# Performance work log

Hardware: AMD Instinct MI355X
Metric: run time of the kernel (lower is better)

Reference implementation:

```python
import jax, jax.numpy as jnp
import numpy as np

N_NODES = 50000
N_EDGES = 600000
D_IN = 128
D_HID = 128
N_IDX = 4096


def gcn_conv(x, W, b, edge_index, num_nodes):
    """PyG GCNConv: add self loops, symmetric deg normalization, scatter-add, bias."""
    h = x @ W  # [N, D_out]
    loop = jnp.arange(num_nodes, dtype=edge_index.dtype)
    src = jnp.concatenate([edge_index[0], loop])
    dst = jnp.concatenate([edge_index[1], loop])
    deg = jax.ops.segment_sum(jnp.ones_like(dst, dtype=h.dtype), dst, num_segments=num_nodes)
    dinv = jnp.where(deg > 0, jax.lax.rsqrt(jnp.maximum(deg, 1.0)), 0.0)
    norm = dinv[src] * dinv[dst]  # [E+N]
    msgs = h[src] * norm[:, None]
    out = jax.ops.segment_sum(msgs, dst, num_segments=num_nodes)
    return out + b


def setup_inputs() -> dict:
    key = jax.random.key(0)
    ks = jax.random.split(key, 18)
    d = {
        "x": jax.random.normal(ks[0], (N_NODES, D_IN), dtype=jnp.float32),
        "syntactic_edge_index": jax.random.randint(ks[1], (2, N_EDGES), 0, N_NODES, dtype=jnp.int32),
        "sequential_edge_index": jax.random.randint(ks[2], (2, N_EDGES), 0, N_NODES, dtype=jnp.int32),
        "semantic_edge_index": jax.random.randint(ks[3], (2, N_EDGES), 0, N_NODES, dtype=jnp.int32),
        "index": jax.random.randint(ks[4], (N_IDX,), 0, N_NODES, dtype=jnp.int32),
    }
    s = 1.0 / np.sqrt(D_IN)
    names = ["syn", "seq", "sem"]
    for i, n in enumerate(names):
        d[f"w1_{n}"] = jax.random.uniform(ks[5 + i], (D_IN, D_HID), jnp.float32, -s, s)
        d[f"b1_{n}"] = jnp.zeros((D_HID,), jnp.float32)
        d[f"w2_{n}"] = jax.random.uniform(ks[8 + i], (D_HID, D_HID), jnp.float32, -s, s)
        d[f"b2_{n}"] = jnp.zeros((D_HID,), jnp.float32)
    return d


def reference(x, syntactic_edge_index, sequential_edge_index, semantic_edge_index, index,
              w1_syn, b1_syn, w1_seq, b1_seq, w1_sem, b1_sem,
              w2_syn, b2_syn, w2_seq, b2_seq, w2_sem, b2_sem):
    n = x.shape[0]
    # layer 1: three parallel GCN branches + ReLU (dropout is identity in eval mode)
    a = jax.nn.relu(gcn_conv(x, w1_syn, b1_syn, syntactic_edge_index, n))
    b = jax.nn.relu(gcn_conv(x, w1_seq, b1_seq, sequential_edge_index, n))
    c = jax.nn.relu(gcn_conv(x, w1_sem, b1_sem, semantic_edge_index, n))
    h = jnp.maximum(jnp.maximum(a, b), c)
    # layer 2
    a2 = jax.nn.relu(gcn_conv(h, w2_syn, b2_syn, syntactic_edge_index, n))
    b2 = jax.nn.relu(gcn_conv(h, w2_seq, b2_seq, sequential_edge_index, n))
    c2 = jax.nn.relu(gcn_conv(h, w2_sem, b2_sem, semantic_edge_index, n))
    out = jnp.maximum(jnp.maximum(a2, b2), c2)
    return out[index]
```

## Files before the change

### kernel.cpp

```cpp
#include <hip/hip_runtime.h>
#include <hip/hip_fp16.h>

#define NN 50000
#define NE 600000
#define NG 3
#define D  128
#define NI 4096
#define BW 1024
#define NBUCK 49
#define CAP 16384
#define REGION (NBUCK * CAP)
#define EPT_BIN 16
#define EPB_BIN (256 * EPT_BIN)
#define NBLK_BIN ((NE + EPB_BIN - 1) / EPB_BIN)
#define XCVT_BLKS 3125
#define WCVT_BLKS 48

typedef _Float16 half8 __attribute__((ext_vector_type(8)));
typedef float floatx4 __attribute__((ext_vector_type(4)));

static __device__ __forceinline__ float wextract(unsigned int v) {
  unsigned short u = (unsigned short)(v >> 16);
  _Float16 h;
  __builtin_memcpy(&h, &u, 2);
  return (float)h;
}

static __device__ __forceinline__ unsigned short h16(float f) {
  _Float16 h = (_Float16)f;
  unsigned short u;
  __builtin_memcpy(&u, &h, 2);
  return u;
}


__global__ __launch_bounds__(256) void prep_kernel(
    const float* __restrict__ x, __half* __restrict__ xh,
    const float* __restrict__ W0, const float* __restrict__ W1, const float* __restrict__ W2,
    const float* __restrict__ W3, const float* __restrict__ W4, const float* __restrict__ W5,
    __half* __restrict__ Wf, int* __restrict__ gcur) {
  int blk = blockIdx.x;
  int tid = threadIdx.x;
  if (blk < XCVT_BLKS) {
    int i = blk * 256 + tid;
    size_t base = (size_t)i * 8;
    float4 v0 = *(const float4*)&x[base];
    float4 v1 = *(const float4*)&x[base + 4];
    half8 h;
    h[0] = (_Float16)v0.x; h[1] = (_Float16)v0.y; h[2] = (_Float16)v0.z; h[3] = (_Float16)v0.w;
    h[4] = (_Float16)v1.x; h[5] = (_Float16)v1.y; h[6] = (_Float16)v1.z; h[7] = (_Float16)v1.w;
    *(half8*)&xh[base] = h;
  } else if (blk < XCVT_BLKS + WCVT_BLKS) {
    const float* Wm[6] = {W0, W1, W2, W3, W4, W5};
    int t = (blk - XCVT_BLKS) * 256 + tid;
    int mat = t >> 11;
    int fr = (t >> 6) & 31;
    int lane = t & 63;
    int tt = fr >> 2, ks = fr & 3;
    int n = tt * 16 + (lane & 15);
    int kb = ks * 32 + (lane >> 4) * 8;
    const float* W = Wm[mat];
#pragma unroll
    for (int j = 0; j < 8; j++)
      Wf[(size_t)t * 8 + j] = __float2half(W[(kb + j) * 128 + n]);
  } else {
    if (tid < NG * NBUCK) gcur[tid] = (tid % NBUCK) * CAP;
  }
}

__global__ __launch_bounds__(256) void bin_kernel(const int* __restrict__ e0,
    const int* __restrict__ e1, const int* __restrict__ e2,
    int* __restrict__ gcur, unsigned int* __restrict__ binned) {
  __shared__ int cnt[4][NBUCK];
  __shared__ int base[NBUCK];
  __shared__ int woff[4][NBUCK];
  int g = blockIdx.y;
  const int* ei = (g == 0) ? e0 : ((g == 1) ? e1 : e2);
  int tid = threadIdx.x;
  int wave = tid >> 6;
  if (tid < NBUCK) { cnt[0][tid] = 0; cnt[1][tid] = 0; cnt[2][tid] = 0; cnt[3][tid] = 0; }
  __syncthreads();
  int estart = blockIdx.x * EPB_BIN;
  int src[EPT_BIN], dst[EPT_BIN], rk[EPT_BIN];
#pragma unroll
  for (int i = 0; i < EPT_BIN; i++) {
    int e = estart + tid + i * 256;
    if (e < NE) {
      src[i] = ei[e];
      dst[i] = ei[NE + e];
      rk[i] = atomicAdd(&cnt[wave][dst[i] >> 10], 1);
    } else {
      rk[i] = -1;
    }
  }
  __syncthreads();
  if (tid < NBUCK) {
    int c0 = cnt[0][tid], c1 = cnt[1][tid], c2 = cnt[2][tid], c3 = cnt[3][tid];
    int total = c0 + c1 + c2 + c3;
    base[tid] = (total > 0) ? atomicAdd(&gcur[g * NBUCK + tid], total) : 0;
    woff[0][tid] = 0; woff[1][tid] = c0; woff[2][tid] = c0 + c1; woff[3][tid] = c0 + c1 + c2;
  }
  __syncthreads();
#pragma unroll
  for (int i = 0; i < EPT_BIN; i++) {
    if (rk[i] >= 0) {
      int b = dst[i] >> 10;
      int pos = base[b] + woff[wave][b] + rk[i];
      if (pos < (b + 1) * CAP)
        binned[(size_t)g * REGION + pos] =
            (unsigned int)src[i] | ((unsigned int)dst[i] << 16);
    }
  }
}

__global__ __launch_bounds__(256) void csr_kernel(const unsigned int* __restrict__ binned,
    const int* __restrict__ gcur, unsigned int* __restrict__ rp32,
    float* __restrict__ dinv, unsigned short* __restrict__ dinvh) {
  __shared__ int deg[BW];
  __shared__ int wsum[4];
  int g = blockIdx.y, b = blockIdx.x;
  int tid = threadIdx.x;
  int node0 = b * BW;
  int cbase = b * CAP;
  int total = min(gcur[g * NBUCK + b] - cbase, CAP);
  const unsigned int* bp = binned + (size_t)g * REGION + cbase;
  for (int i = tid; i < BW; i += 256) deg[i] = 0;
  __syncthreads();
  for (int e = tid; e < total; e += 256) {
    unsigned int p = bp[e];
    atomicAdd(&deg[(int)(p >> 16) - node0], 1);
  }
  __syncthreads();
  int d0 = deg[tid * 4], d1 = deg[tid * 4 + 1], d2 = deg[tid * 4 + 2], d3 = deg[tid * 4 + 3];
  int s = d0 + d1 + d2 + d3;
  int lane = tid & 63;
  int incl = s;
#pragma unroll
  for (int off = 1; off < 64; off <<= 1) {
    int n = __shfl_up(incl, off, 64);
    if (lane >= off) incl += n;
  }
  if (lane == 63) wsum[tid >> 6] = incl;
  __syncthreads();
  int wbase = 0;
#pragma unroll
  for (int w = 0; w < 4; w++)
    if (w < (tid >> 6)) wbase += wsum[w];
  int ex = wbase + incl - s;
  int exs[4] = {ex, ex + d0, ex + d0 + d1, ex + d0 + d1 + d2};
  int ds[4] = {d0, d1, d2, d3};
#pragma unroll
  for (int k = 0; k < 4; k++) {
    int node = node0 + tid * 4 + k;
    if (node < NN) {
      unsigned int st = (unsigned int)(cbase + exs[k]);
      rp32[g * NN + node] = st | ((unsigned int)ds[k] << 20);
      float di = rsqrtf((float)ds[k] + 1.0f);
      dinv[g * NN + node] = di;
      dinvh[g * NN + node] = h16(di);
    }
  }
}

__global__ __launch_bounds__(256) void fillp_kernel(const unsigned int* __restrict__ binned,
    const int* __restrict__ gcur, const unsigned int* __restrict__ rp32,
    const unsigned short* __restrict__ dinvh, unsigned int* __restrict__ colp) {
  __shared__ int cur[BW];
  int g = blockIdx.y, b = blockIdx.x;
  int tid = threadIdx.x;
  int node0 = b * BW;
  int cbase = b * CAP;
  int total = min(gcur[g * NBUCK + b] - cbase, CAP);
  const unsigned int* bp = binned + (size_t)g * REGION + cbase;
  for (int i = tid; i < BW; i += 256) {
    int node = node0 + i;
    cur[i] = (node < NN) ? (int)(rp32[g * NN + node] & 0xFFFFFu) : 0;
  }
  __syncthreads();
  const unsigned short* dh = dinvh + (size_t)g * NN;
  unsigned int* cg = colp + (size_t)g * REGION;
  for (int e = tid; e < total; e += 256) {
    unsigned int p = bp[e];
    int srcid = (int)(p & 0xffffu);
    int r = atomicAdd(&cur[(int)(p >> 16) - node0], 1);
    cg[r] = (unsigned int)srcid | ((unsigned int)dh[srcid] << 16);
  }
}


__global__ __launch_bounds__(256) void aggb_kernel(
    const __half* __restrict__ srch, const unsigned int* __restrict__ rp32,
    const unsigned int* __restrict__ colp, const float* __restrict__ dinv,
    const int* __restrict__ index, __half* __restrict__ tout, int nrows) {
  int b = blockIdx.y;
  int lane = threadIdx.x & 63;
  int grp = lane >> 4;
  int l16 = lane & 15;
  int gb = grp << 4;
  int wv = (blockIdx.x * 256 + threadIdx.x) >> 6;
  int w = wv * 4 + grp;
  int valid = (w < nrows);
  int wc = valid ? w : 0;
  int node = index ? index[wc] : wc;
  const _Float16* srcv = (const _Float16*)srch;
  unsigned int r32 = rp32[(size_t)b * NN + node];
  int s = (int)(r32 & 0xFFFFFu);
  int n = valid ? (int)(r32 >> 20) : 0;
  float di = dinv[b * NN + node];
  half8 selfh = *(const half8*)&srcv[(size_t)node * D + l16 * 8];
  float a[8];
#pragma unroll
  for (int k = 0; k < 8; k++) a[k] = di * (float)selfh[k];
  int nmax = n;
  nmax = max(nmax, __shfl_xor(nmax, 16, 64));
  nmax = max(nmax, __shfl_xor(nmax, 32, 64));
  const unsigned int* cp = colp + (size_t)b * REGION;
  for (int j0 = 0; j0 < nmax; j0 += 16) {
    unsigned int c = (j0 + l16 < n) ? cp[s + j0 + l16] : 0u;
    int rem = nmax - j0;
    rem = (rem > 16) ? 16 : rem;
    for (int jj = 0; jj < rem; jj += 4) {
      unsigned int v0 = (unsigned int)__shfl((int)c, gb + jj + 0, 64);
      unsigned int v1 = (unsigned int)__shfl((int)c, gb + jj + 1, 64);
      unsigned int v2 = (unsigned int)__shfl((int)c, gb + jj + 2, 64);
      unsigned int v3 = (unsigned int)__shfl((int)c, gb + jj + 3, 64);
      half8 h0 = *(const half8*)&srcv[(size_t)(v0 & 0xffffu) * D + l16 * 8];
      half8 h1 = *(const half8*)&srcv[(size_t)(v1 & 0xffffu) * D + l16 * 8];
      half8 h2 = *(const half8*)&srcv[(size_t)(v2 & 0xffffu) * D + l16 * 8];
      half8 h3 = *(const half8*)&srcv[(size_t)(v3 & 0xffffu) * D + l16 * 8];
      float w0 = wextract(v0), w1 = wextract(v1);
      float w2 = wextract(v2), w3 = wextract(v3);
#pragma unroll
      for (int k = 0; k < 8; k++) a[k] = fmaf((float)h0[k], w0, a[k]);
#pragma unroll
      for (int k = 0; k < 8; k++) a[k] = fmaf((float)h1[k], w1, a[k]);
#pragma unroll
      for (int k = 0; k < 8; k++) a[k] = fmaf((float)h2[k], w2, a[k]);
#pragma unroll
      for (int k = 0; k < 8; k++) a[k] = fmaf((float)h3[k], w3, a[k]);
    }
  }
  if (valid) {
    half8 o;
#pragma unroll
    for (int k = 0; k < 8; k++) o[k] = (_Float16)(di * a[k]);
    _Float16* tv = (_Float16*)tout;
    *(half8*)&tv[(size_t)b * nrows * D + (size_t)w * D + l16 * 8] = o;
  }
}


#define ALD 136

__global__ __launch_bounds__(256) void mmf_kernel(const __half* __restrict__ A,
    const __half* __restrict__ Wf,
    const float* __restrict__ B0, const float* __restrict__ B1, const float* __restrict__ B2,
    __half* __restrict__ outh, float* __restrict__ outf, int M) {
  __shared__ _Float16 As[128 * ALD];
  __shared__ _Float16 Ws[16384];
  const float* Bb[3] = {B0, B1, B2};
  const int tid = threadIdx.x;
  const int wave = tid >> 6, lane = tid & 63;
  const int wr = (wave >> 1) * 64, wc = (wave & 1) * 64;
  const int ln = lane & 15, quad = lane >> 4;
  const int row0 = blockIdx.x * 128;
  float om[4][4][4];

  for (int b = 0; b < 3; b++) {
    const __half* Wb = Wf + (size_t)b * 16384;
#pragma unroll
    for (int i = 0; i < 8; i++) {
      int id = tid + i * 256;
      *(half8*)&Ws[id * 8] = *(const half8*)&Wb[(size_t)id * 8];
    }
    const __half* Ab = A + (size_t)b * M * D;
#pragma unroll
    for (int i = 0; i < 8; i++) {
      int idx = tid + i * 256;
      int r = idx >> 4, c8 = idx & 15;
      int gr = row0 + r;
      gr = (gr < M) ? gr : (M - 1);
      half8 v = *(const half8*)&Ab[(size_t)gr * D + c8 * 8];
      *(half8*)&As[r * ALD + c8 * 8] = v;
    }
    __syncthreads();

    float bias[4];
#pragma unroll
    for (int ct = 0; ct < 4; ct++) bias[ct] = Bb[b][wc + ct * 16 + ln];
    floatx4 acc[4][4];
#pragma unroll
    for (int rt = 0; rt < 4; rt++)
#pragma unroll
      for (int ct = 0; ct < 4; ct++)
        acc[rt][ct] = (floatx4){bias[ct], bias[ct], bias[ct], bias[ct]};

#pragma unroll
    for (int ks = 0; ks < 4; ks++) {
      half8 av[4];
#pragma unroll
      for (int rt = 0; rt < 4; rt++)
        av[rt] = *(const half8*)&As[(wr + rt * 16 + ln) * ALD + ks * 32 + quad * 8];
#pragma unroll
      for (int ct = 0; ct < 4; ct++) {
        int tt = (wc >> 4) + ct;
        half8 bv = *(const half8*)&Ws[((tt * 4 + ks) * 64 + lane) * 8];
#pragma unroll
        for (int rt = 0; rt < 4; rt++)
          acc[rt][ct] = __builtin_amdgcn_mfma_f32_16x16x32_f16(av[rt], bv, acc[rt][ct], 0, 0, 0);
      }
    }
#pragma unroll
    for (int rt = 0; rt < 4; rt++)
#pragma unroll
      for (int ct = 0; ct < 4; ct++)
#pragma unroll
        for (int r = 0; r < 4; r++) {
          float v = fmaxf(acc[rt][ct][r], 0.f);
          om[rt][ct][r] = (b == 0) ? v : fmaxf(om[rt][ct][r], v);
        }
    __syncthreads();
  }
#pragma unroll
  for (int rt = 0; rt < 4; rt++) {
    int m = row0 + wr + rt * 16 + quad * 4;
#pragma unroll
    for (int r = 0; r < 4; r++) {
      if (m + r < M) {
#pragma unroll
        for (int ct = 0; ct < 4; ct++) {
          int n = wc + ct * 16 + ln;
          if (outh) outh[(size_t)(m + r) * D + n] = __float2half(om[rt][ct][r]);
          else      outf[(size_t)(m + r) * D + n] = om[rt][ct][r];
        }
      }
    }
  }
}


extern "C" void kernel_launch(void* const* d_in, const int* in_sizes, int n_in,
                              void* d_out, int out_size, void* d_ws, size_t ws_size,
                              hipStream_t stream) {
  const float* x = (const float*)d_in[0];
  const int* e0 = (const int*)d_in[1];
  const int* e1 = (const int*)d_in[2];
  const int* e2 = (const int*)d_in[3];
  const int* index = (const int*)d_in[4];
  const float* w1[3] = {(const float*)d_in[5], (const float*)d_in[9],  (const float*)d_in[13]};
  const float* b1[3] = {(const float*)d_in[6], (const float*)d_in[10], (const float*)d_in[14]};
  const float* w2[3] = {(const float*)d_in[7], (const float*)d_in[11], (const float*)d_in[15]};
  const float* b2[3] = {(const float*)d_in[8], (const float*)d_in[12], (const float*)d_in[16]};
  float* out = (float*)d_out;

  char* ws = (char*)d_ws;
  size_t o = 0;
  auto alloc = [&](size_t bytes) {
    o = (o + 255) & ~(size_t)255;
    void* p = ws + o;
    o += bytes;
    return p;
  };
  unsigned int* rp32 = (unsigned int*)alloc((size_t)NG * NN * 4);
  unsigned int* colp = (unsigned int*)alloc((size_t)NG * REGION * 4);
  float*  dinv   = (float*)alloc((size_t)NG * NN * 4);
  unsigned short* dinvh = (unsigned short*)alloc((size_t)NG * NN * 2);
  int*    gcur   = (int*)alloc((size_t)NG * NBUCK * 4);
  __half* xh     = (__half*)alloc((size_t)NN * D * 2);
  __half* Wf     = (__half*)alloc((size_t)6 * 128 * 128 * 2);
  __half* t1     = (__half*)alloc((size_t)NG * NN * D * 2);
  __half* hacc   = (__half*)alloc((size_t)NN * D * 2);
  unsigned int* binned = (unsigned int*)t1;
  __half* t2     = t1;
  (void)ws_size; (void)in_sizes; (void)n_in; (void)out_size;

  prep_kernel<<<XCVT_BLKS + WCVT_BLKS + 1, 256, 0, stream>>>(
      x, xh, w1[0], w1[1], w1[2], w2[0], w2[1], w2[2], Wf, gcur);
  bin_kernel<<<dim3(NBLK_BIN, NG), 256, 0, stream>>>(e0, e1, e2, gcur, binned);
  csr_kernel<<<dim3(NBUCK, NG), 256, 0, stream>>>(binned, gcur, rp32, dinv, dinvh);
  fillp_kernel<<<dim3(NBUCK, NG), 256, 0, stream>>>(binned, gcur, rp32, dinvh, colp);

  aggb_kernel<<<dim3((NN + 15) / 16, NG), 256, 0, stream>>>(
      xh, rp32, colp, dinv, nullptr, t1, NN);
  mmf_kernel<<<(NN + 127) / 128, 256, 0, stream>>>(t1, Wf, b1[0], b1[1], b1[2],
                                                   hacc, nullptr, NN);
  aggb_kernel<<<dim3((NI + 15) / 16, NG), 256, 0, stream>>>(
      hacc, rp32, colp, dinv, index, t2, NI);
  mmf_kernel<<<(NI + 127) / 128, 256, 0, stream>>>(t2, Wf + (size_t)3 * 16384,
                                                   b2[0], b2[1], b2[2], nullptr, out, NI);
}
```

Baseline: 261.9 us.

## Fuse layer-1 aggregation and matmul into one kernel per 128-row tile

Replaces the separate layer-1 aggregation kernel and MFMA matmul kernel with a single kernel. Each 512-thread block gathers neighbour features for 128 rows of each graph into shared memory, multiplies by that graph's weights with MFMA, and keeps a running max across the three branches. This removes the round trip of the 3×N×D fp16 intermediate through global memory and one launch. The cost is lower parallelism in the gather phase, only 391 blocks, and load imbalance from degree variation inside each block, serialized by barriers between gather and matmul.

```diff
diff --git a/kernel.cpp b/kernel.cpp
--- a/kernel.cpp
+++ b/kernel.cpp
@@ -187,6 +187,132 @@
   }
 }
 
+#define ALD 136
+
+__global__ __launch_bounds__(512, 4) void flayer_kernel(
+    const __half* __restrict__ srch, const unsigned int* __restrict__ rp32,
+    const unsigned int* __restrict__ colp, const float* __restrict__ dinv,
+    const __half* __restrict__ Wf,
+    const float* __restrict__ B0, const float* __restrict__ B1, const float* __restrict__ B2,
+    __half* __restrict__ outh, int M) {
+  __shared__ _Float16 As[128 * ALD];
+  __shared__ _Float16 Ws[16384];
+  const float* Bb[3] = {B0, B1, B2};
+  const int tid = threadIdx.x;
+  const int wave = tid >> 6, lane = tid & 63;
+  const int grp = lane >> 4;
+  const int l16 = lane & 15;
+  const int gb = grp << 4;
+  const int wr = (wave >> 2) * 64, wc = (wave & 3) * 32;
+  const int row0 = blockIdx.x * 128;
+  const _Float16* srcv = (const _Float16*)srch;
+  float om[4][2][4];
+
+  for (int b = 0; b < 3; b++) {
+    const __half* Wb = Wf + (size_t)b * 16384;
+#pragma unroll
+    for (int i = 0; i < 4; i++) {
+      int id = tid + i * 512;
+      *(half8*)&Ws[id * 8] = *(const half8*)&Wb[(size_t)id * 8];
+    }
+    const unsigned int* cp = colp + (size_t)b * REGION;
+    for (int it = 0; it < 4; it++) {
+      int r = it * 32 + wave * 4 + grp;
+      int w = row0 + r;
+      int node = (w < M) ? w : (M - 1);
+      unsigned int r32 = rp32[(size_t)b * NN + node];
+      int s = (int)(r32 & 0xFFFFFu);
+      int n = (int)(r32 >> 20);
+      float di = dinv[b * NN + node];
+      half8 selfh = *(const half8*)&srcv[(size_t)node * D + l16 * 8];
+      float a[8];
+#pragma unroll
+      for (int k = 0; k < 8; k++) a[k] = di * (float)selfh[k];
+      int nmax = n;
+      nmax = max(nmax, __shfl_xor(nmax, 16, 64));
+      nmax = max(nmax, __shfl_xor(nmax, 32, 64));
+      for (int j0 = 0; j0 < nmax; j0 += 16) {
+        unsigned int c = (j0 + l16 < n) ? __builtin_nontemporal_load(&cp[s + j0 + l16]) : 0u;
+        int rem = nmax - j0;
+        rem = (rem > 16) ? 16 : rem;
+        for (int jj = 0; jj < rem; jj += 4) {
+          unsigned int v0 = (unsigned int)__shfl((int)c, gb + jj + 0, 64);
+          unsigned int v1 = (unsigned int)__shfl((int)c, gb + jj + 1, 64);
+          unsigned int v2 = (unsigned int)__shfl((int)c, gb + jj + 2, 64);
+          unsigned int v3 = (unsigned int)__shfl((int)c, gb + jj + 3, 64);
+          half8 h0 = *(const half8*)&srcv[(size_t)(v0 & 0xffffu) * D + l16 * 8];
+          half8 h1 = *(const half8*)&srcv[(size_t)(v1 & 0xffffu) * D + l16 * 8];
+          half8 h2 = *(const half8*)&srcv[(size_t)(v2 & 0xffffu) * D + l16 * 8];
+          half8 h3 = *(const half8*)&srcv[(size_t)(v3 & 0xffffu) * D + l16 * 8];
+          float w0 = wextract(v0), w1 = wextract(v1);
+          float w2 = wextract(v2), w3 = wextract(v3);
+#pragma unroll
+          for (int k = 0; k < 8; k++) a[k] = fmaf((float)h0[k], w0, a[k]);
+#pragma unroll
+          for (int k = 0; k < 8; k++) a[k] = fmaf((float)h1[k], w1, a[k]);
+#pragma unroll
+          for (int k = 0; k < 8; k++) a[k] = fmaf((float)h2[k], w2, a[k]);
+#pragma unroll
+          for (int k = 0; k < 8; k++) a[k] = fmaf((float)h3[k], w3, a[k]);
+        }
+      }
+      half8 o;
+#pragma unroll
+      for (int k = 0; k < 8; k++) o[k] = (_Float16)(di * a[k]);
+      *(half8*)&As[r * ALD + l16 * 8] = o;
+    }
+    __syncthreads();
+
+    float bias[2];
+#pragma unroll
+    for (int ct = 0; ct < 2; ct++) bias[ct] = Bb[b][wc + ct * 16 + l16];
+    floatx4 acc[4][2];
+#pragma unroll
+    for (int rt = 0; rt < 4; rt++)
+#pragma unroll
+      for (int ct = 0; ct < 2; ct++)
+        acc[rt][ct] = (floatx4){bias[ct], bias[ct], bias[ct], bias[ct]};
+#pragma unroll
+    for (int ks = 0; ks < 4; ks++) {
+      half8 av[4];
+#pragma unroll
+      for (int rt = 0; rt < 4; rt++)
+        av[rt] = *(const half8*)&As[(wr + rt * 16 + l16) * ALD + ks * 32 + grp * 8];
+#pragma unroll
+      for (int ct = 0; ct < 2; ct++) {
+        int tt = (wc >> 4) + ct;
+        half8 bv = *(const half8*)&Ws[((tt * 4 + ks) * 64 + lane) * 8];
+#pragma unroll
+        for (int rt = 0; rt < 4; rt++)
+          acc[rt][ct] = __builtin_amdgcn_mfma_f32_16x16x32_f16(av[rt], bv, acc[rt][ct], 0, 0, 0);
+      }
+    }
+#pragma unroll
+    for (int rt = 0; rt < 4; rt++)
+#pragma unroll
+      for (int ct = 0; ct < 2; ct++)
+#pragma unroll
+        for (int r = 0; r < 4; r++) {
+          float v = fmaxf(acc[rt][ct][r], 0.f);
+          om[rt][ct][r] = (b == 0) ? v : fmaxf(om[rt][ct][r], v);
+        }
+    __syncthreads();
+  }
+#pragma unroll
+  for (int rt = 0; rt < 4; rt++) {
+    int m = row0 + wr + rt * 16 + grp * 4;
+#pragma unroll
+    for (int r = 0; r < 4; r++) {
+      if (m + r < M) {
+#pragma unroll
+        for (int ct = 0; ct < 2; ct++) {
+          int n = wc + ct * 16 + l16;
+          outh[(size_t)(m + r) * D + n] = __float2half(om[rt][ct][r]);
+        }
+      }
+    }
+  }
+}
 
 __global__ __launch_bounds__(256) void aggb_kernel(
     const __half* __restrict__ srch, const unsigned int* __restrict__ rp32,
@@ -250,8 +376,6 @@
 }
 
 
-#define ALD 136
-
 __global__ __launch_bounds__(256) void mmf_kernel(const __half* __restrict__ A,
     const __half* __restrict__ Wf,
     const float* __restrict__ B0, const float* __restrict__ B1, const float* __restrict__ B2,
@@ -368,10 +492,9 @@
   int*    gcur   = (int*)alloc((size_t)NG * NBUCK * 4);
   __half* xh     = (__half*)alloc((size_t)NN * D * 2);
   __half* Wf     = (__half*)alloc((size_t)6 * 128 * 128 * 2);
-  __half* t1     = (__half*)alloc((size_t)NG * NN * D * 2);
+  unsigned int* binned = (unsigned int*)alloc((size_t)NG * REGION * 4);
   __half* hacc   = (__half*)alloc((size_t)NN * D * 2);
-  unsigned int* binned = (unsigned int*)t1;
-  __half* t2     = t1;
+  __half* t2     = (__half*)binned;
   (void)ws_size; (void)in_sizes; (void)n_in; (void)out_size;
 
   prep_kernel<<<XCVT_BLKS + WCVT_BLKS + 1, 256, 0, stream>>>(
@@ -380,10 +503,8 @@
   csr_kernel<<<dim3(NBUCK, NG), 256, 0, stream>>>(binned, gcur, rp32, dinv, dinvh);
   fillp_kernel<<<dim3(NBUCK, NG), 256, 0, stream>>>(binned, gcur, rp32, dinvh, colp);
 
-  aggb_kernel<<<dim3((NN + 15) / 16, NG), 256, 0, stream>>>(
-      xh, rp32, colp, dinv, nullptr, t1, NN);
-  mmf_kernel<<<(NN + 127) / 128, 256, 0, stream>>>(t1, Wf, b1[0], b1[1], b1[2],
-                                                   hacc, nullptr, NN);
+  flayer_kernel<<<(NN + 127) / 128, 512, 0, stream>>>(
+      xh, rp32, colp, dinv, Wf, b1[0], b1[1], b1[2], hacc, NN);
   aggb_kernel<<<dim3((NI + 15) / 16, NG), 256, 0, stream>>>(
       hacc, rp32, colp, dinv, index, t2, NI);
   mmf_kernel<<<(NI + 127) / 128, 256, 0, stream>>>(t2, Wf + (size_t)3 * 16384,
```

Result: no change. 265.7 us (+1.5%).

## Fuse preprocessing, binning, CSR build and fill into one cooperative kernel

Applied to the files above, without the earlier changes.

Merges the four preprocessing kernels (x/W conversion, edge binning, CSR degree scan, column fill) into a single cooperative launch separated by grid-wide syncs. The x conversion becomes a grid-stride loop over the smaller grid of 441 blocks (147 per graph). The aim is to remove three kernel launch boundaries and their gaps. The trade-off is grid.sync cost, fewer blocks doing the x conversion, and phases that use only 147 of the blocks while the rest sit idle.

```diff
diff --git a/kernel.cpp b/kernel.cpp
--- a/kernel.cpp
+++ b/kernel.cpp
@@ -1,5 +1,8 @@
 #include <hip/hip_runtime.h>
 #include <hip/hip_fp16.h>
+#include <hip/hip_cooperative_groups.h>
+
+namespace cg = cooperative_groups;
 
 #define NN 50000
 #define NE 600000
@@ -13,8 +16,7 @@
 #define EPT_BIN 16
 #define EPB_BIN (256 * EPT_BIN)
 #define NBLK_BIN ((NE + EPB_BIN - 1) / EPB_BIN)
-#define XCVT_BLKS 3125
-#define WCVT_BLKS 48
+#define CGRID (NBLK_BIN * NG)
 
 typedef _Float16 half8 __attribute__((ext_vector_type(8)));
 typedef float floatx4 __attribute__((ext_vector_type(4)));
@@ -34,15 +36,26 @@
 }
 
 
-__global__ __launch_bounds__(256) void prep_kernel(
+__global__ __launch_bounds__(256) void coop_prep_kernel(
     const float* __restrict__ x, __half* __restrict__ xh,
     const float* __restrict__ W0, const float* __restrict__ W1, const float* __restrict__ W2,
     const float* __restrict__ W3, const float* __restrict__ W4, const float* __restrict__ W5,
-    __half* __restrict__ Wf, int* __restrict__ gcur) {
-  int blk = blockIdx.x;
-  int tid = threadIdx.x;
-  if (blk < XCVT_BLKS) {
-    int i = blk * 256 + tid;
+    __half* __restrict__ Wf, int* __restrict__ gcur,
+    const int* __restrict__ e0, const int* __restrict__ e1, const int* __restrict__ e2,
+    unsigned int* __restrict__ binned, unsigned int* __restrict__ rp32,
+    float* __restrict__ dinv, unsigned short* __restrict__ dinvh,
+    unsigned int* __restrict__ colp) {
+  cg::grid_group grid = cg::this_grid();
+  __shared__ int s_cnt[4][NBUCK];
+  __shared__ int s_base[NBUCK];
+  __shared__ int s_woff[4][NBUCK];
+  __shared__ int s_arr[BW];
+  __shared__ int s_wsum[4];
+  const int blk = blockIdx.x;
+  const int tid = threadIdx.x;
+  const int t = blk * 256 + tid;
+
+  for (int i = t; i < NN * D / 8; i += CGRID * 256) {
     size_t base = (size_t)i * 8;
     float4 v0 = *(const float4*)&x[base];
     float4 v1 = *(const float4*)&x[base + 4];
@@ -50,9 +63,9 @@
     h[0] = (_Float16)v0.x; h[1] = (_Float16)v0.y; h[2] = (_Float16)v0.z; h[3] = (_Float16)v0.w;
     h[4] = (_Float16)v1.x; h[5] = (_Float16)v1.y; h[6] = (_Float16)v1.z; h[7] = (_Float16)v1.w;
     *(half8*)&xh[base] = h;
-  } else if (blk < XCVT_BLKS + WCVT_BLKS) {
+  }
+  if (t < 6 * 2048) {
     const float* Wm[6] = {W0, W1, W2, W3, W4, W5};
-    int t = (blk - XCVT_BLKS) * 256 + tid;
     int mat = t >> 11;
     int fr = (t >> 6) & 31;
     int lane = t & 63;
@@ -63,127 +76,115 @@
 #pragma unroll
     for (int j = 0; j < 8; j++)
       Wf[(size_t)t * 8 + j] = __float2half(W[(kb + j) * 128 + n]);
-  } else {
-    if (tid < NG * NBUCK) gcur[tid] = (tid % NBUCK) * CAP;
-  }
-}
-
-__global__ __launch_bounds__(256) void bin_kernel(const int* __restrict__ e0,
-    const int* __restrict__ e1, const int* __restrict__ e2,
-    int* __restrict__ gcur, unsigned int* __restrict__ binned) {
-  __shared__ int cnt[4][NBUCK];
-  __shared__ int base[NBUCK];
-  __shared__ int woff[4][NBUCK];
-  int g = blockIdx.y;
-  const int* ei = (g == 0) ? e0 : ((g == 1) ? e1 : e2);
-  int tid = threadIdx.x;
-  int wave = tid >> 6;
-  if (tid < NBUCK) { cnt[0][tid] = 0; cnt[1][tid] = 0; cnt[2][tid] = 0; cnt[3][tid] = 0; }
-  __syncthreads();
-  int estart = blockIdx.x * EPB_BIN;
-  int src[EPT_BIN], dst[EPT_BIN], rk[EPT_BIN];
-#pragma unroll
-  for (int i = 0; i < EPT_BIN; i++) {
-    int e = estart + tid + i * 256;
-    if (e < NE) {
-      src[i] = ei[e];
-      dst[i] = ei[NE + e];
-      rk[i] = atomicAdd(&cnt[wave][dst[i] >> 10], 1);
-    } else {
-      rk[i] = -1;
-    }
-  }
-  __syncthreads();
-  if (tid < NBUCK) {
-    int c0 = cnt[0][tid], c1 = cnt[1][tid], c2 = cnt[2][tid], c3 = cnt[3][tid];
-    int total = c0 + c1 + c2 + c3;
-    base[tid] = (total > 0) ? atomicAdd(&gcur[g * NBUCK + tid], total) : 0;
-    woff[0][tid] = 0; woff[1][tid] = c0; woff[2][tid] = c0 + c1; woff[3][tid] = c0 + c1 + c2;
-  }
-  __syncthreads();
-#pragma unroll
-  for (int i = 0; i < EPT_BIN; i++) {
-    if (rk[i] >= 0) {
-      int b = dst[i] >> 10;
-      int pos = base[b] + woff[wave][b] + rk[i];
-      if (pos < (b + 1) * CAP)
-        binned[(size_t)g * REGION + pos] =
-            (unsigned int)src[i] | ((unsigned int)dst[i] << 16);
-    }
-  }
-}
-
-__global__ __launch_bounds__(256) void csr_kernel(const unsigned int* __restrict__ binned,
-    const int* __restrict__ gcur, unsigned int* __restrict__ rp32,
-    float* __restrict__ dinv, unsigned short* __restrict__ dinvh) {
-  __shared__ int deg[BW];
-  __shared__ int wsum[4];
-  int g = blockIdx.y, b = blockIdx.x;
-  int tid = threadIdx.x;
-  int node0 = b * BW;
-  int cbase = b * CAP;
-  int total = min(gcur[g * NBUCK + b] - cbase, CAP);
-  const unsigned int* bp = binned + (size_t)g * REGION + cbase;
-  for (int i = tid; i < BW; i += 256) deg[i] = 0;
-  __syncthreads();
-  for (int e = tid; e < total; e += 256) {
-    unsigned int p = bp[e];
-    atomicAdd(&deg[(int)(p >> 16) - node0], 1);
-  }
-  __syncthreads();
-  int d0 = deg[tid * 4], d1 = deg[tid * 4 + 1], d2 = deg[tid * 4 + 2], d3 = deg[tid * 4 + 3];
-  int s = d0 + d1 + d2 + d3;
-  int lane = tid & 63;
-  int incl = s;
-#pragma unroll
-  for (int off = 1; off < 64; off <<= 1) {
-    int n = __shfl_up(incl, off, 64);
-    if (lane >= off) incl += n;
-  }
-  if (lane == 63) wsum[tid >> 6] = incl;
-  __syncthreads();
-  int wbase = 0;
-#pragma unroll
-  for (int w = 0; w < 4; w++)
-    if (w < (tid >> 6)) wbase += wsum[w];
-  int ex = wbase + incl - s;
-  int exs[4] = {ex, ex + d0, ex + d0 + d1, ex + d0 + d1 + d2};
-  int ds[4] = {d0, d1, d2, d3};
-#pragma unroll
-  for (int k = 0; k < 4; k++) {
-    int node = node0 + tid * 4 + k;
-    if (node < NN) {
-      unsigned int st = (unsigned int)(cbase + exs[k]);
-      rp32[g * NN + node] = st | ((unsigned int)ds[k] << 20);
-      float di = rsqrtf((float)ds[k] + 1.0f);
-      dinv[g * NN + node] = di;
-      dinvh[g * NN + node] = h16(di);
-    }
-  }
-}
-
-__global__ __launch_bounds__(256) void fillp_kernel(const unsigned int* __restrict__ binned,
-    const int* __restrict__ gcur, const unsigned int* __restrict__ rp32,
-    const unsigned short* __restrict__ dinvh, unsigned int* __restrict__ colp) {
-  __shared__ int cur[BW];
-  int g = blockIdx.y, b = blockIdx.x;
-  int tid = threadIdx.x;
-  int node0 = b * BW;
-  int cbase = b * CAP;
-  int total = min(gcur[g * NBUCK + b] - cbase, CAP);
-  const unsigned int* bp = binned + (size_t)g * REGION + cbase;
-  for (int i = tid; i < BW; i += 256) {
-    int node = node0 + i;
-    cur[i] = (node < NN) ? (int)(rp32[g * NN + node] & 0xFFFFFu) : 0;
-  }
-  __syncthreads();
-  const unsigned short* dh = dinvh + (size_t)g * NN;
-  unsigned int* cg = colp + (size_t)g * REGION;
-  for (int e = tid; e < total; e += 256) {
-    unsigned int p = bp[e];
-    int srcid = (int)(p & 0xffffu);
-    int r = atomicAdd(&cur[(int)(p >> 16) - node0], 1);
-    cg[r] = (unsigned int)srcid | ((unsigned int)dh[srcid] << 16);
+  }
+  if (t < NG * NBUCK) gcur[t] = (t % NBUCK) * CAP;
+  grid.sync();
+
+  {
+    int g = blk / NBLK_BIN, eb = blk % NBLK_BIN;
+    const int* ei = (g == 0) ? e0 : ((g == 1) ? e1 : e2);
+    int wave = tid >> 6;
+    if (tid < NBUCK) { s_cnt[0][tid] = 0; s_cnt[1][tid] = 0; s_cnt[2][tid] = 0; s_cnt[3][tid] = 0; }
+    __syncthreads();
+    int estart = eb * EPB_BIN;
+    int src[EPT_BIN], dst[EPT_BIN], rk[EPT_BIN];
+#pragma unroll
+    for (int i = 0; i < EPT_BIN; i++) {
+      int e = estart + tid + i * 256;
+      if (e < NE) {
+        src[i] = ei[e];
+        dst[i] = ei[NE + e];
+        rk[i] = atomicAdd(&s_cnt[wave][dst[i] >> 10], 1);
+      } else {
+        rk[i] = -1;
+      }
+    }
+    __syncthreads();
+    if (tid < NBUCK) {
+      int c0 = s_cnt[0][tid], c1 = s_cnt[1][tid], c2 = s_cnt[2][tid], c3 = s_cnt[3][tid];
+      int total = c0 + c1 + c2 + c3;
+      s_base[tid] = (total > 0) ? atomicAdd(&gcur[g * NBUCK + tid], total) : 0;
+      s_woff[0][tid] = 0; s_woff[1][tid] = c0; s_woff[2][tid] = c0 + c1; s_woff[3][tid] = c0 + c1 + c2;
+    }
+    __syncthreads();
+#pragma unroll
+    for (int i = 0; i < EPT_BIN; i++) {
+      if (rk[i] >= 0) {
+        int b = dst[i] >> 10;
+        int pos = s_base[b] + s_woff[wave][b] + rk[i];
+        if (pos < (b + 1) * CAP)
+          binned[(size_t)g * REGION + pos] =
+              (unsigned int)src[i] | ((unsigned int)dst[i] << 16);
+      }
+    }
+  }
+  grid.sync();
+
+  if (blk < NG * NBUCK) {
+    int g = blk / NBUCK, b = blk % NBUCK;
+    int node0 = b * BW;
+    int cbase = b * CAP;
+    int total = min(gcur[g * NBUCK + b] - cbase, CAP);
+    const unsigned int* bp = binned + (size_t)g * REGION + cbase;
+    for (int i = tid; i < BW; i += 256) s_arr[i] = 0;
+    __syncthreads();
+    for (int e = tid; e < total; e += 256) {
+      unsigned int p = bp[e];
+      atomicAdd(&s_arr[(int)(p >> 16) - node0], 1);
+    }
+    __syncthreads();
+    int d0 = s_arr[tid * 4], d1 = s_arr[tid * 4 + 1];
+    int d2 = s_arr[tid * 4 + 2], d3 = s_arr[tid * 4 + 3];
+    int s = d0 + d1 + d2 + d3;
+    int lane = tid & 63;
+    int incl = s;
+#pragma unroll
+    for (int off = 1; off < 64; off <<= 1) {
+      int n = __shfl_up(incl, off, 64);
+      if (lane >= off) incl += n;
+    }
+    if (lane == 63) s_wsum[tid >> 6] = incl;
+    __syncthreads();
+    int wbase = 0;
+#pragma unroll
+    for (int w = 0; w < 4; w++)
+      if (w < (tid >> 6)) wbase += s_wsum[w];
+    int ex = wbase + incl - s;
+    int exs[4] = {ex, ex + d0, ex + d0 + d1, ex + d0 + d1 + d2};
+    int ds[4] = {d0, d1, d2, d3};
+#pragma unroll
+    for (int k = 0; k < 4; k++) {
+      int node = node0 + tid * 4 + k;
+      if (node < NN) {
+        unsigned int st = (unsigned int)(cbase + exs[k]);
+        rp32[g * NN + node] = st | ((unsigned int)ds[k] << 20);
+        float di = rsqrtf((float)ds[k] + 1.0f);
+        dinv[g * NN + node] = di;
+        dinvh[g * NN + node] = h16(di);
+      }
+    }
+  }
+  grid.sync();
+
+  if (blk < NG * NBUCK) {
+    int g = blk / NBUCK, b = blk % NBUCK;
+    int node0 = b * BW;
+    int cbase = b * CAP;
+    int total = min(gcur[g * NBUCK + b] - cbase, CAP);
+    const unsigned int* bp = binned + (size_t)g * REGION + cbase;
+    for (int i = tid; i < BW; i += 256) {
+      int node = node0 + i;
+      s_arr[i] = (node < NN) ? (int)(rp32[g * NN + node] & 0xFFFFFu) : 0;
+    }
+    __syncthreads();
+    const unsigned short* dh = dinvh + (size_t)g * NN;
+    unsigned int* cg_ = colp + (size_t)g * REGION;
+    for (int e = tid; e < total; e += 256) {
+      unsigned int p = bp[e];
+      int srcid = (int)(p & 0xffffu);
+      int r = atomicAdd(&s_arr[(int)(p >> 16) - node0], 1);
+      cg_[r] = (unsigned int)srcid | ((unsigned int)dh[srcid] << 16);
+    }
   }
 }
 
@@ -374,11 +375,18 @@
   __half* t2     = t1;
   (void)ws_size; (void)in_sizes; (void)n_in; (void)out_size;
 
-  prep_kernel<<<XCVT_BLKS + WCVT_BLKS + 1, 256, 0, stream>>>(
-      x, xh, w1[0], w1[1], w1[2], w2[0], w2[1], w2[2], Wf, gcur);
-  bin_kernel<<<dim3(NBLK_BIN, NG), 256, 0, stream>>>(e0, e1, e2, gcur, binned);
-  csr_kernel<<<dim3(NBUCK, NG), 256, 0, stream>>>(binned, gcur, rp32, dinv, dinvh);
-  fillp_kernel<<<dim3(NBUCK, NG), 256, 0, stream>>>(binned, gcur, rp32, dinvh, colp);
+  {
+    const float* W0 = w1[0]; const float* W1 = w1[1]; const float* W2 = w1[2];
+    const float* W3 = w2[0]; const float* W4 = w2[1]; const float* W5 = w2[2];
+    void* cargs[] = {
+        (void*)&x, (void*)&xh,
+        (void*)&W0, (void*)&W1, (void*)&W2, (void*)&W3, (void*)&W4, (void*)&W5,
+        (void*)&Wf, (void*)&gcur,
+        (void*)&e0, (void*)&e1, (void*)&e2,
+        (void*)&binned, (void*)&rp32, (void*)&dinv, (void*)&dinvh, (void*)&colp};
+    hipLaunchCooperativeKernel((const void*)coop_prep_kernel,
+                               dim3(CGRID), dim3(256), cargs, 0, stream);
+  }
 
   aggb_kernel<<<dim3((NN + 15) / 16, NG), 256, 0, stream>>>(
       xh, rp32, colp, dinv, nullptr, t1, NN);
```

Result: slower. 454.9 us (+73.7%).

## Fuse prep with binning and CSR with fill, gather dinv in aggregation

Applied to the files above, without the earlier changes.

Merges the x/W conversion kernel into the edge-binning kernel, which now uses a grid-stride loop for the conversion, and merges the CSR offset build with the column fill so the scanned offsets are reused from shared memory. The gcur counters are now zeroed with a memset and hold per-bucket offsets. Column entries no longer pack the source's half-precision dinv; the aggregation kernel gathers dinvh[src] per neighbor and masks padded lanes. This cuts kernel launches and one pass over binned edges, at the cost of an extra dependent gather per neighbor in the aggregation hot loop.

```diff
diff --git a/kernel.cpp b/kernel.cpp
--- a/kernel.cpp
+++ b/kernel.cpp
@@ -13,18 +13,11 @@
 #define EPT_BIN 16
 #define EPB_BIN (256 * EPT_BIN)
 #define NBLK_BIN ((NE + EPB_BIN - 1) / EPB_BIN)
-#define XCVT_BLKS 3125
-#define WCVT_BLKS 48
+#define PB_GRID (NBLK_BIN * NG)
+#define XCVT_TOT (NN * D / 8)
 
 typedef _Float16 half8 __attribute__((ext_vector_type(8)));
 typedef float floatx4 __attribute__((ext_vector_type(4)));
-
-static __device__ __forceinline__ float wextract(unsigned int v) {
-  unsigned short u = (unsigned short)(v >> 16);
-  _Float16 h;
-  __builtin_memcpy(&h, &u, 2);
-  return (float)h;
-}
 
 static __device__ __forceinline__ unsigned short h16(float f) {
   _Float16 h = (_Float16)f;
@@ -34,25 +27,31 @@
 }
 
 
-__global__ __launch_bounds__(256) void prep_kernel(
+__global__ __launch_bounds__(256) void prepbin_kernel(
     const float* __restrict__ x, __half* __restrict__ xh,
     const float* __restrict__ W0, const float* __restrict__ W1, const float* __restrict__ W2,
     const float* __restrict__ W3, const float* __restrict__ W4, const float* __restrict__ W5,
-    __half* __restrict__ Wf, int* __restrict__ gcur) {
-  int blk = blockIdx.x;
-  int tid = threadIdx.x;
-  if (blk < XCVT_BLKS) {
-    int i = blk * 256 + tid;
-    size_t base = (size_t)i * 8;
-    float4 v0 = *(const float4*)&x[base];
-    float4 v1 = *(const float4*)&x[base + 4];
+    __half* __restrict__ Wf,
+    const int* __restrict__ e0, const int* __restrict__ e1, const int* __restrict__ e2,
+    int* __restrict__ gcur, unsigned int* __restrict__ binned) {
+  __shared__ int cnt[4][NBUCK];
+  __shared__ int base[NBUCK];
+  __shared__ int woff[4][NBUCK];
+  const int blk = blockIdx.x;
+  const int tid = threadIdx.x;
+  const int t = blk * 256 + tid;
+
+  for (int i = t; i < XCVT_TOT; i += PB_GRID * 256) {
+    size_t base8 = (size_t)i * 8;
+    float4 v0 = *(const float4*)&x[base8];
+    float4 v1 = *(const float4*)&x[base8 + 4];
     half8 h;
     h[0] = (_Float16)v0.x; h[1] = (_Float16)v0.y; h[2] = (_Float16)v0.z; h[3] = (_Float16)v0.w;
     h[4] = (_Float16)v1.x; h[5] = (_Float16)v1.y; h[6] = (_Float16)v1.z; h[7] = (_Float16)v1.w;
-    *(half8*)&xh[base] = h;
-  } else if (blk < XCVT_BLKS + WCVT_BLKS) {
+    *(half8*)&xh[base8] = h;
+  }
+  if (t < 6 * 2048) {
     const float* Wm[6] = {W0, W1, W2, W3, W4, W5};
-    int t = (blk - XCVT_BLKS) * 256 + tid;
     int mat = t >> 11;
     int fr = (t >> 6) & 31;
     int lane = t & 63;
@@ -63,24 +62,14 @@
 #pragma unroll
     for (int j = 0; j < 8; j++)
       Wf[(size_t)t * 8 + j] = __float2half(W[(kb + j) * 128 + n]);
-  } else {
-    if (tid < NG * NBUCK) gcur[tid] = (tid % NBUCK) * CAP;
-  }
-}
-
-__global__ __launch_bounds__(256) void bin_kernel(const int* __restrict__ e0,
-    const int* __restrict__ e1, const int* __restrict__ e2,
-    int* __restrict__ gcur, unsigned int* __restrict__ binned) {
-  __shared__ int cnt[4][NBUCK];
-  __shared__ int base[NBUCK];
-  __shared__ int woff[4][NBUCK];
-  int g = blockIdx.y;
+  }
+
+  int g = blk / NBLK_BIN, eb = blk % NBLK_BIN;
   const int* ei = (g == 0) ? e0 : ((g == 1) ? e1 : e2);
-  int tid = threadIdx.x;
   int wave = tid >> 6;
   if (tid < NBUCK) { cnt[0][tid] = 0; cnt[1][tid] = 0; cnt[2][tid] = 0; cnt[3][tid] = 0; }
   __syncthreads();
-  int estart = blockIdx.x * EPB_BIN;
+  int estart = eb * EPB_BIN;
   int src[EPT_BIN], dst[EPT_BIN], rk[EPT_BIN];
 #pragma unroll
   for (int i = 0; i < EPT_BIN; i++) {
@@ -105,33 +94,34 @@
   for (int i = 0; i < EPT_BIN; i++) {
     if (rk[i] >= 0) {
       int b = dst[i] >> 10;
-      int pos = base[b] + woff[wave][b] + rk[i];
-      if (pos < (b + 1) * CAP)
-        binned[(size_t)g * REGION + pos] =
+      int ofs = base[b] + woff[wave][b] + rk[i];
+      if (ofs < CAP)
+        binned[(size_t)g * REGION + b * CAP + ofs] =
             (unsigned int)src[i] | ((unsigned int)dst[i] << 16);
     }
   }
 }
 
-__global__ __launch_bounds__(256) void csr_kernel(const unsigned int* __restrict__ binned,
-    const int* __restrict__ gcur, unsigned int* __restrict__ rp32,
-    float* __restrict__ dinv, unsigned short* __restrict__ dinvh) {
-  __shared__ int deg[BW];
+__global__ __launch_bounds__(256) void csrfill_kernel(
+    const unsigned int* __restrict__ binned, const int* __restrict__ gcur,
+    unsigned int* __restrict__ rp32, float* __restrict__ dinv,
+    unsigned short* __restrict__ dinvh, unsigned int* __restrict__ colp) {
+  __shared__ int arr[BW];
   __shared__ int wsum[4];
   int g = blockIdx.y, b = blockIdx.x;
   int tid = threadIdx.x;
   int node0 = b * BW;
   int cbase = b * CAP;
-  int total = min(gcur[g * NBUCK + b] - cbase, CAP);
+  int total = min(gcur[g * NBUCK + b], CAP);
   const unsigned int* bp = binned + (size_t)g * REGION + cbase;
-  for (int i = tid; i < BW; i += 256) deg[i] = 0;
+  for (int i = tid; i < BW; i += 256) arr[i] = 0;
   __syncthreads();
   for (int e = tid; e < total; e += 256) {
     unsigned int p = bp[e];
-    atomicAdd(&deg[(int)(p >> 16) - node0], 1);
-  }
-  __syncthreads();
-  int d0 = deg[tid * 4], d1 = deg[tid * 4 + 1], d2 = deg[tid * 4 + 2], d3 = deg[tid * 4 + 3];
+    atomicAdd(&arr[(int)(p >> 16) - node0], 1);
+  }
+  __syncthreads();
+  int d0 = arr[tid * 4], d1 = arr[tid * 4 + 1], d2 = arr[tid * 4 + 2], d3 = arr[tid * 4 + 3];
   int s = d0 + d1 + d2 + d3;
   int lane = tid & 63;
   int incl = s;
@@ -152,38 +142,21 @@
 #pragma unroll
   for (int k = 0; k < 4; k++) {
     int node = node0 + tid * 4 + k;
+    int st = cbase + exs[k];
     if (node < NN) {
-      unsigned int st = (unsigned int)(cbase + exs[k]);
-      rp32[g * NN + node] = st | ((unsigned int)ds[k] << 20);
+      rp32[g * NN + node] = (unsigned int)st | ((unsigned int)ds[k] << 20);
       float di = rsqrtf((float)ds[k] + 1.0f);
       dinv[g * NN + node] = di;
       dinvh[g * NN + node] = h16(di);
     }
-  }
-}
-
-__global__ __launch_bounds__(256) void fillp_kernel(const unsigned int* __restrict__ binned,
-    const int* __restrict__ gcur, const unsigned int* __restrict__ rp32,
-    const unsigned short* __restrict__ dinvh, unsigned int* __restrict__ colp) {
-  __shared__ int cur[BW];
-  int g = blockIdx.y, b = blockIdx.x;
-  int tid = threadIdx.x;
-  int node0 = b * BW;
-  int cbase = b * CAP;
-  int total = min(gcur[g * NBUCK + b] - cbase, CAP);
-  const unsigned int* bp = binned + (size_t)g * REGION + cbase;
-  for (int i = tid; i < BW; i += 256) {
-    int node = node0 + i;
-    cur[i] = (node < NN) ? (int)(rp32[g * NN + node] & 0xFFFFFu) : 0;
-  }
-  __syncthreads();
-  const unsigned short* dh = dinvh + (size_t)g * NN;
+    arr[tid * 4 + k] = st;
+  }
+  __syncthreads();
   unsigned int* cg = colp + (size_t)g * REGION;
   for (int e = tid; e < total; e += 256) {
     unsigned int p = bp[e];
-    int srcid = (int)(p & 0xffffu);
-    int r = atomicAdd(&cur[(int)(p >> 16) - node0], 1);
-    cg[r] = (unsigned int)srcid | ((unsigned int)dh[srcid] << 16);
+    int r = atomicAdd(&arr[(int)(p >> 16) - node0], 1);
+    cg[r] = p & 0xffffu;
   }
 }
 
@@ -191,6 +164,7 @@
 __global__ __launch_bounds__(256) void aggb_kernel(
     const __half* __restrict__ srch, const unsigned int* __restrict__ rp32,
     const unsigned int* __restrict__ colp, const float* __restrict__ dinv,
+    const unsigned short* __restrict__ dinvh,
     const int* __restrict__ index, __half* __restrict__ tout, int nrows) {
   int b = blockIdx.y;
   int lane = threadIdx.x & 63;
@@ -203,6 +177,7 @@
   int wc = valid ? w : 0;
   int node = index ? index[wc] : wc;
   const _Float16* srcv = (const _Float16*)srch;
+  const _Float16* dh = (const _Float16*)dinvh + (size_t)b * NN;
   unsigned int r32 = rp32[(size_t)b * NN + node];
   int s = (int)(r32 & 0xFFFFFu);
   int n = valid ? (int)(r32 >> 20) : 0;
@@ -224,12 +199,14 @@
       unsigned int v1 = (unsigned int)__shfl((int)c, gb + jj + 1, 64);
       unsigned int v2 = (unsigned int)__shfl((int)c, gb + jj + 2, 64);
       unsigned int v3 = (unsigned int)__shfl((int)c, gb + jj + 3, 64);
-      half8 h0 = *(const half8*)&srcv[(size_t)(v0 & 0xffffu) * D + l16 * 8];
-      half8 h1 = *(const half8*)&srcv[(size_t)(v1 & 0xffffu) * D + l16 * 8];
-      half8 h2 = *(const half8*)&srcv[(size_t)(v2 & 0xffffu) * D + l16 * 8];
-      half8 h3 = *(const half8*)&srcv[(size_t)(v3 & 0xffffu) * D + l16 * 8];
-      float w0 = wextract(v0), w1 = wextract(v1);
-      float w2 = wextract(v2), w3 = wextract(v3);
+      half8 h0 = *(const half8*)&srcv[(size_t)v0 * D + l16 * 8];
+      half8 h1 = *(const half8*)&srcv[(size_t)v1 * D + l16 * 8];
+      half8 h2 = *(const half8*)&srcv[(size_t)v2 * D + l16 * 8];
+      half8 h3 = *(const half8*)&srcv[(size_t)v3 * D + l16 * 8];
+      float w0 = (j0 + jj + 0 < n) ? (float)dh[v0] : 0.f;
+      float w1 = (j0 + jj + 1 < n) ? (float)dh[v1] : 0.f;
+      float w2 = (j0 + jj + 2 < n) ? (float)dh[v2] : 0.f;
+      float w3 = (j0 + jj + 3 < n) ? (float)dh[v3] : 0.f;
 #pragma unroll
       for (int k = 0; k < 8; k++) a[k] = fmaf((float)h0[k], w0, a[k]);
 #pragma unroll
@@ -374,18 +351,17 @@
   __half* t2     = t1;
   (void)ws_size; (void)in_sizes; (void)n_in; (void)out_size;
 
-  prep_kernel<<<XCVT_BLKS + WCVT_BLKS + 1, 256, 0, stream>>>(
-      x, xh, w1[0], w1[1], w1[2], w2[0], w2[1], w2[2], Wf, gcur);
-  bin_kernel<<<dim3(NBLK_BIN, NG), 256, 0, stream>>>(e0, e1, e2, gcur, binned);
-  csr_kernel<<<dim3(NBUCK, NG), 256, 0, stream>>>(binned, gcur, rp32, dinv, dinvh);
-  fillp_kernel<<<dim3(NBUCK, NG), 256, 0, stream>>>(binned, gcur, rp32, dinvh, colp);
+  hipMemsetAsync(gcur, 0, (size_t)NG * NBUCK * 4, stream);
+  prepbin_kernel<<<PB_GRID, 256, 0, stream>>>(
+      x, xh, w1[0], w1[1], w1[2], w2[0], w2[1], w2[2], Wf, e0, e1, e2, gcur, binned);
+  csrfill_kernel<<<dim3(NBUCK, NG), 256, 0, stream>>>(binned, gcur, rp32, dinv, dinvh, colp);
 
   aggb_kernel<<<dim3((NN + 15) / 16, NG), 256, 0, stream>>>(
-      xh, rp32, colp, dinv, nullptr, t1, NN);
+      xh, rp32, colp, dinv, dinvh, nullptr, t1, NN);
   mmf_kernel<<<(NN + 127) / 128, 256, 0, stream>>>(t1, Wf, b1[0], b1[1], b1[2],
                                                    hacc, nullptr, NN);
   aggb_kernel<<<dim3((NI + 15) / 16, NG), 256, 0, stream>>>(
-      hacc, rp32, colp, dinv, index, t2, NI);
+      hacc, rp32, colp, dinv, dinvh, index, t2, NI);
   mmf_kernel<<<(NI + 127) / 128, 256, 0, stream>>>(t2, Wf + (size_t)3 * 16384,
                                                    b2[0], b2[1], b2[2], nullptr, out, NI);
 }
```

Measured after the change: 265.7 us. No clear change (+1.5%).
